# Optimization experiments

Measured on AMD Instinct MI355X. Metric: run time of the kernel, lower is better.

The kernel has to match this reference:

```python
import jax, jax.numpy as jnp
import numpy as np

B, H, P, D = 32, 8, 16, 32
OUT_DIM = 32
GROUPS = 64
NUM_F = 8
N = H * P * D                 # 4096 (self.num)
PHO = P * H * OUT_DIM         # 4096


def setup_inputs() -> dict:
    key = jax.random.key(0)
    ks = jax.random.split(key, 10)
    return {
        "q": jax.random.normal(ks[0], (B, H, P, D), dtype=jnp.float32),
        "k": jax.random.normal(ks[1], (B, H, P, D), dtype=jnp.float32),
        "grid": jnp.arange(NUM_F, dtype=jnp.float32) + 1.0,
        "base_weight_q": jax.random.uniform(ks[2], (PHO, N), dtype=jnp.float32),
        "base_weight_k": jax.random.uniform(ks[3], (PHO, N), dtype=jnp.float32),
        "coef_q": jax.random.uniform(ks[4], (GROUPS, 1, NUM_F), dtype=jnp.float32),
        "coef_k": jax.random.uniform(ks[5], (GROUPS, 1, NUM_F), dtype=jnp.float32),
        # grouped 1x1 conv == num_f independent [PHO, N] matmuls (only conv_layer_q is used in forward)
        "conv_wq": jax.random.normal(ks[6], (NUM_F, PHO, N), dtype=jnp.float32) * 0.01,
        "conv_bq": jax.random.normal(ks[7], (NUM_F, PHO), dtype=jnp.float32) * 0.01,
        "scale_sp": jnp.ones((PHO,), dtype=jnp.float32),
    }


def reference(q, k, grid, base_weight_q, base_weight_k, coef_q, coef_k, conv_wq, conv_bq, scale_sp):
    b, h, p, d = q.shape
    n = h * p * d
    nf = grid.shape[0]
    gs = n // coef_q.shape[0]               # group_size
    out_dim = base_weight_q.shape[0] // (p * h)

    qf = q.reshape(b, n)
    kf = k.reshape(b, n)

    base_q = jax.nn.silu(qf) @ base_weight_q.T          # [B, PHO]
    base_k = jax.nn.silu(kf) @ base_weight_k.T

    # per-feature coef: feature i in group i//gs, scaled per frequency f -> [F, N]
    ce_q = jnp.repeat(coef_q[:, 0, :], gs, axis=0).T
    ce_k = jnp.repeat(coef_k[:, 0, :], gs, axis=0).T

    sq = jnp.sin(grid[None, :, None] * qf[:, None, :]) * ce_q[None]   # [B, F, N]
    sk = jnp.sin(grid[None, :, None] * kf[:, None, :]) * ce_k[None]

    # grouped conv1d (kernel 1, groups=num_f): per-frequency matmul; original uses conv_layer_q for both
    fq = jnp.einsum('bfn,fon->bfo', sq, conv_wq) + conv_bq[None]      # [B, F, PHO]
    fq = fq.sum(axis=1) * scale_sp
    fk = jnp.einsum('bfn,fon->bfo', sk, conv_wq) + conv_bq[None]
    fk = fk.sum(axis=1) * scale_sp

    y = (fq * scale_sp + base_q) + (fk * scale_sp + base_k)
    y = y.reshape(b, h, p, out_dim)
    return jax.nn.softmax(y, axis=-1)
```

## Files before the change

kernel.cpp:

```cpp
#include <hip/hip_runtime.h>
#include <math.h>

#define N_TOT 4096
#define PHO_T 4096
#define KTOT  40960
#define NS    2560

typedef __attribute__((ext_vector_type(8)))  short short8v;
typedef __attribute__((ext_vector_type(16))) float f32x16;

#define GLD16(src, dst) __builtin_amdgcn_global_load_lds(                      \
    (const __attribute__((address_space(1))) void*)(src),                      \
    (__attribute__((address_space(3))) void*)(dst), 16, 0, 0)

__device__ __forceinline__ void split1(float x, short& h, short& l) {
    unsigned u  = __builtin_bit_cast(unsigned, x);
    unsigned hu = (u + 0x7FFFu + ((u >> 16) & 1u)) & 0xFFFF0000u;
    h = (short)(hu >> 16);
    float r = x - __builtin_bit_cast(float, hu);
    unsigned ur = __builtin_bit_cast(unsigned, r);
    l = (short)((ur + 0x7FFFu + ((ur >> 16) & 1u)) >> 16);
}

__global__ void act_kernel(const float* __restrict__ q,
                           const float* __restrict__ kx,
                           const float* __restrict__ grid_,
                           const float* __restrict__ coefq,
                           const float* __restrict__ coefk,
                           short* __restrict__ Af)
{
    const int t = blockIdx.x * 256 + threadIdx.x;
    const int S = t >> 6;
    const int l = t & 63;
    const int b = l & 31;
    const int k0 = S * 16 + (l >> 5) * 8;

    float v[8];
    if (k0 < 8192) {
        const float* src = (k0 < 4096) ? (q  + (size_t)b * N_TOT + k0)
                                       : (kx + (size_t)b * N_TOT + (k0 - 4096));
#pragma unroll
        for (int j = 0; j < 8; ++j) {
            const float x = src[j];
            v[j] = x / (1.f + __expf(-x));
        }
    } else {
        const int f  = (k0 - 8192) >> 12;
        const int n0 = (k0 - 8192) & 4095;
        const int g  = n0 >> 6;
        const float gf  = grid_[f];
        const float cq_ = coefq[g * 8 + f];
        const float ck_ = coefk[g * 8 + f];
        const float* qp = q  + (size_t)b * N_TOT + n0;
        const float* kp = kx + (size_t)b * N_TOT + n0;
#pragma unroll
        for (int j = 0; j < 8; ++j)
            v[j] = sinf(gf * qp[j]) * cq_ + sinf(gf * kp[j]) * ck_;
    }

    short8v hi, lo;
#pragma unroll
    for (int j = 0; j < 8; ++j) { short h, lw; split1(v[j], h, lw); hi[j] = h; lo[j] = lw; }
    *(short8v*)&Af[((size_t)(S * 2 + 0) * 64 + l) * 8] = hi;
    *(short8v*)&Af[((size_t)(S * 2 + 1) * 64 + l) * 8] = lo;
}

__global__ void init_kernel(const float* __restrict__ cb,
                            const float* __restrict__ ssp,
                            float* __restrict__ ypre)
{
    const int t = blockIdx.x * 256 + threadIdx.x;
    const int o = t & 4095;
    const float s = ssp[o];
    float acc = 0.f;
#pragma unroll
    for (int f = 0; f < 8; ++f) acc += cb[f * PHO_T + o];
    ypre[t] = 2.f * s * s * acc;
}

#define OBK  256
#define KC   32
#define NCH  8

__global__ __launch_bounds__(256) void gemm_kernel(
    const float* __restrict__ bwq, const float* __restrict__ bwk,
    const float* __restrict__ cw,  const short* __restrict__ Af,
    const float* __restrict__ ssp, float* __restrict__ ypre)
{
    __shared__ float Wl[2][OBK * KC];

    const int t  = threadIdx.x;
    const int ks = blockIdx.x >> 4;
    const int ob = blockIdx.x & 15;
    const int o_base = ob * OBK;

    const float* Wp;
    int s_base;
    bool scaled;
    if (ks < 16) {
        Wp = bwq + ks * 256;
        s_base = ks * 16;
        scaled = false;
    } else if (ks < 32) {
        Wp = bwk + (ks - 16) * 256;
        s_base = 256 + (ks - 16) * 16;
        scaled = false;
    } else {
        const int c2 = ks - 32;
        const int f  = c2 >> 4;
        const int noff = (c2 & 15) * 256;
        Wp = cw + (size_t)f * (size_t)PHO_T * N_TOT + noff;
        s_base = 512 + f * 256 + (c2 & 15) * 16;
        scaled = true;
    }

    const int w  = t >> 6;
    const int l  = t & 63;
    const int srow  = l >> 3;
    const int sslot = (l & 7) ^ (srow & 7);

    f32x16 acc0, acc1;
#pragma unroll
    for (int i = 0; i < 16; ++i) { acc0[i] = 0.f; acc1[i] = 0.f; }

    auto stage = [&](int c, int buf) {
        const int k0 = c * KC;
#pragma unroll
        for (int i = 0; i < 8; ++i) {
            const int row = w * 64 + i * 8 + srow;
            const float* src = Wp + (size_t)(o_base + row) * N_TOT + k0 + sslot * 4;
            GLD16(src, &Wl[buf][(w * 64 + i * 8) * KC]);
        }
    };

    stage(0, 0);
    __syncthreads();

    const int rkey = l & 7;
    const int row0 = w * 64 + (l & 31);

    for (int c = 0; c < NCH; ++c) {
        const int cur = c & 1;
        if (c + 1 < NCH) stage(c + 1, cur ^ 1);

#pragma unroll
        for (int s = 0; s < 2; ++s) {
            const size_t Sg = (size_t)(s_base + c * 2 + s);
            const short8v ah = *(const short8v*)&Af[((Sg * 2 + 0) * 64 + l) * 8];
            const short8v al = *(const short8v*)&Af[((Sg * 2 + 1) * 64 + l) * 8];
            const int j0 = s * 4 + (l >> 5) * 2;

            auto tileop = [&](int nt, f32x16& acc) {
                const float* rp = &Wl[cur][(row0 + nt * 32) * KC];
                const float4 wa = *(const float4*)&rp[((j0    ) ^ rkey) * 4];
                const float4 wb = *(const float4*)&rp[((j0 + 1) ^ rkey) * 4];
                short8v bh, bl;
                {
                    short h, lw;
                    split1(wa.x, h, lw); bh[0] = h; bl[0] = lw;
                    split1(wa.y, h, lw); bh[1] = h; bl[1] = lw;
                    split1(wa.z, h, lw); bh[2] = h; bl[2] = lw;
                    split1(wa.w, h, lw); bh[3] = h; bl[3] = lw;
                    split1(wb.x, h, lw); bh[4] = h; bl[4] = lw;
                    split1(wb.y, h, lw); bh[5] = h; bl[5] = lw;
                    split1(wb.z, h, lw); bh[6] = h; bl[6] = lw;
                    split1(wb.w, h, lw); bh[7] = h; bl[7] = lw;
                }
                acc = __builtin_amdgcn_mfma_f32_32x32x16_bf16(ah, bh, acc, 0, 0, 0);
                acc = __builtin_amdgcn_mfma_f32_32x32x16_bf16(ah, bl, acc, 0, 0, 0);
                acc = __builtin_amdgcn_mfma_f32_32x32x16_bf16(al, bh, acc, 0, 0, 0);
            };
            tileop(0, acc0);
            tileop(1, acc1);
        }
        __syncthreads();
    }

    const int o0 = o_base + w * 64 + (l & 31);
    const int o1 = o0 + 32;
    float s0 = 1.f, s1 = 1.f;
    if (scaled) {
        const float x0 = ssp[o0], x1 = ssp[o1];
        s0 = x0 * x0; s1 = x1 * x1;
    }
    const int bh4 = 4 * (l >> 5);
#pragma unroll
    for (int r = 0; r < 16; ++r) {
        const int b = (r & 3) + 8 * (r >> 2) + bh4;
        atomicAdd(&ypre[(size_t)b * PHO_T + o0], acc0[r] * s0);
        atomicAdd(&ypre[(size_t)b * PHO_T + o1], acc1[r] * s1);
    }
}

__global__ void softmax_kernel(const float* __restrict__ yp,
                               float* __restrict__ out)
{
    const int t  = threadIdx.x;
    const int r  = blockIdx.x * 8 + (t >> 5);
    const int od = t & 31;
    const float v = yp[(size_t)r * 32 + od];
    float m = v;
#pragma unroll
    for (int s = 16; s > 0; s >>= 1) m = fmaxf(m, __shfl_xor(m, s, 32));
    const float e = __expf(v - m);
    float sum = e;
#pragma unroll
    for (int s = 16; s > 0; s >>= 1) sum += __shfl_xor(sum, s, 32);
    out[(size_t)r * 32 + od] = e / sum;
}

extern "C" void kernel_launch(void* const* d_in, const int* in_sizes, int n_in,
                              void* d_out, int out_size, void* d_ws, size_t ws_size,
                              hipStream_t stream)
{
    const float* q    = (const float*)d_in[0];
    const float* k    = (const float*)d_in[1];
    const float* grid = (const float*)d_in[2];
    const float* bwq  = (const float*)d_in[3];
    const float* bwk  = (const float*)d_in[4];
    const float* cq   = (const float*)d_in[5];
    const float* ck   = (const float*)d_in[6];
    const float* cw   = (const float*)d_in[7];
    const float* cb   = (const float*)d_in[8];
    const float* ssp  = (const float*)d_in[9];
    float* out = (float*)d_out;

    short* Af   = (short*)d_ws;
    float* ypre = (float*)((char*)d_ws + (size_t)NS * 2 * 64 * 16);

    act_kernel<<<640, 256, 0, stream>>>(q, k, grid, cq, ck, Af);
    init_kernel<<<512, 256, 0, stream>>>(cb, ssp, ypre);
    gemm_kernel<<<2560, 256, 0, stream>>>(bwq, bwk, cw, Af, ssp, ypre);
    softmax_kernel<<<512, 256, 0, stream>>>(ypre, out);
}
```

Measured before the change: 168.9 us.

## Lengthen split-K chunks to cut GEMM block count and atomic traffic

```diff
diff --git a/kernel.cpp b/kernel.cpp
--- a/kernel.cpp
+++ b/kernel.cpp
@@ -80,7 +80,8 @@
 
 #define OBK  256
 #define KC   32
-#define NCH  8
+#define KSUP 1280
+#define NCH  (KSUP / KC)
 
 __global__ __launch_bounds__(256) void gemm_kernel(
     const float* __restrict__ bwq, const float* __restrict__ bwk,
@@ -93,47 +94,38 @@
     const int ks = blockIdx.x >> 4;
     const int ob = blockIdx.x & 15;
     const int o_base = ob * OBK;
-
-    const float* Wp;
-    int s_base;
-    bool scaled;
-    if (ks < 16) {
-        Wp = bwq + ks * 256;
-        s_base = ks * 16;
-        scaled = false;
-    } else if (ks < 32) {
-        Wp = bwk + (ks - 16) * 256;
-        s_base = 256 + (ks - 16) * 16;
-        scaled = false;
-    } else {
-        const int c2 = ks - 32;
-        const int f  = c2 >> 4;
-        const int noff = (c2 & 15) * 256;
-        Wp = cw + (size_t)f * (size_t)PHO_T * N_TOT + noff;
-        s_base = 512 + f * 256 + (c2 & 15) * 16;
-        scaled = true;
-    }
+    const int k_base = ks * KSUP;
 
     const int w  = t >> 6;
     const int l  = t & 63;
     const int srow  = l >> 3;
     const int sslot = (l & 7) ^ (srow & 7);
 
-    f32x16 acc0, acc1;
-#pragma unroll
-    for (int i = 0; i < 16; ++i) { acc0[i] = 0.f; acc1[i] = 0.f; }
-
-    auto stage = [&](int c, int buf) {
-        const int k0 = c * KC;
+    f32x16 accU0, accU1, accS0, accS1;
+#pragma unroll
+    for (int i = 0; i < 16; ++i) {
+        accU0[i] = 0.f; accU1[i] = 0.f; accS0[i] = 0.f; accS1[i] = 0.f;
+    }
+
+    auto wptr = [&](int kg) -> const float* {
+        if (kg < 4096)  return bwq + kg;
+        if (kg < 8192)  return bwk + (kg - 4096);
+        const int f    = (kg - 8192) >> 12;
+        const int noff = (kg - 8192) & 4095;
+        return cw + (size_t)f * (size_t)PHO_T * N_TOT + noff;
+    };
+
+    auto stage = [&](int kg, int buf) {
+        const float* Wp = wptr(kg);
 #pragma unroll
         for (int i = 0; i < 8; ++i) {
             const int row = w * 64 + i * 8 + srow;
-            const float* src = Wp + (size_t)(o_base + row) * N_TOT + k0 + sslot * 4;
+            const float* src = Wp + (size_t)(o_base + row) * N_TOT + sslot * 4;
             GLD16(src, &Wl[buf][(w * 64 + i * 8) * KC]);
         }
     };
 
-    stage(0, 0);
+    stage(k_base, 0);
     __syncthreads();
 
     const int rkey = l & 7;
@@ -141,11 +133,13 @@
 
     for (int c = 0; c < NCH; ++c) {
         const int cur = c & 1;
-        if (c + 1 < NCH) stage(c + 1, cur ^ 1);
-
+        const int kg  = k_base + c * KC;
+        if (c + 1 < NCH) stage(kg + KC, cur ^ 1);
+
+        const bool sc = (kg >= 8192);
 #pragma unroll
         for (int s = 0; s < 2; ++s) {
-            const size_t Sg = (size_t)(s_base + c * 2 + s);
+            const size_t Sg = (size_t)(kg >> 4) + s;
             const short8v ah = *(const short8v*)&Af[((Sg * 2 + 0) * 64 + l) * 8];
             const short8v al = *(const short8v*)&Af[((Sg * 2 + 1) * 64 + l) * 8];
             const int j0 = s * 4 + (l >> 5) * 2;
@@ -170,25 +164,22 @@
                 acc = __builtin_amdgcn_mfma_f32_32x32x16_bf16(ah, bl, acc, 0, 0, 0);
                 acc = __builtin_amdgcn_mfma_f32_32x32x16_bf16(al, bh, acc, 0, 0, 0);
             };
-            tileop(0, acc0);
-            tileop(1, acc1);
+            if (sc) { tileop(0, accS0); tileop(1, accS1); }
+            else    { tileop(0, accU0); tileop(1, accU1); }
         }
         __syncthreads();
     }
 
     const int o0 = o_base + w * 64 + (l & 31);
     const int o1 = o0 + 32;
-    float s0 = 1.f, s1 = 1.f;
-    if (scaled) {
-        const float x0 = ssp[o0], x1 = ssp[o1];
-        s0 = x0 * x0; s1 = x1 * x1;
-    }
+    const float x0 = ssp[o0], x1 = ssp[o1];
+    const float s0 = x0 * x0, s1 = x1 * x1;
     const int bh4 = 4 * (l >> 5);
 #pragma unroll
     for (int r = 0; r < 16; ++r) {
         const int b = (r & 3) + 8 * (r >> 2) + bh4;
-        atomicAdd(&ypre[(size_t)b * PHO_T + o0], acc0[r] * s0);
-        atomicAdd(&ypre[(size_t)b * PHO_T + o1], acc1[r] * s1);
+        atomicAdd(&ypre[(size_t)b * PHO_T + o0], accU0[r] + accS0[r] * s0);
+        atomicAdd(&ypre[(size_t)b * PHO_T + o1], accU1[r] + accS1[r] * s1);
     }
 }
 
@@ -230,6 +221,6 @@
 
     act_kernel<<<640, 256, 0, stream>>>(q, k, grid, cq, ck, Af);
     init_kernel<<<512, 256, 0, stream>>>(cb, ssp, ypre);
-    gemm_kernel<<<2560, 256, 0, stream>>>(bwq, bwk, cw, Af, ssp, ypre);
+    gemm_kernel<<<512, 256, 0, stream>>>(bwq, bwk, cw, Af, ssp, ypre);
     softmax_kernel<<<512, 256, 0, stream>>>(ypre, out);
 }
```

Result: faster. 160.9 us (-4.8%).
